# Optimization experiments

Hardware: AMD Instinct MI355X
Metric: run time of the kernel (lower is better)

## Reference

```python
import jax, jax.numpy as jnp
import numpy as np

N = 50000        # nodes
E = 800000       # edges
G = 256          # graphs in batch
NUM_EMB = 100    # atomic number vocab
D = 64           # atom_emb_dim (node channel dim, constant across layers)
ED = 50          # edge_dim
H = 128          # hidden_dim
L = 4            # num_conv_layers
Z = 2 * D + ED   # CGConv concat dim = 178


def setup_inputs() -> dict:
    key = jax.random.key(0)
    ks = jax.random.split(key, 12)
    x = jax.random.randint(ks[0], (N,), 0, NUM_EMB)
    edge_index = jax.random.randint(ks[1], (2, E), 0, N)
    edge_attr = jax.random.normal(ks[2], (E, ED), dtype=jnp.float32)
    batch = jnp.sort(jax.random.randint(ks[3], (N,), 0, G))
    emb = jax.random.normal(ks[4], (NUM_EMB, D), dtype=jnp.float32) * 0.1
    Wf = jax.random.normal(ks[5], (L, Z, D), dtype=jnp.float32) * (Z ** -0.5)
    bf = jnp.zeros((L, D), jnp.float32)
    Ws = jax.random.normal(ks[6], (L, Z, D), dtype=jnp.float32) * (Z ** -0.5)
    bs = jnp.zeros((L, D), jnp.float32)
    W1 = jax.random.normal(ks[7], (D, H), dtype=jnp.float32) * (D ** -0.5)
    b1 = jnp.zeros((H,), jnp.float32)
    W2 = jax.random.normal(ks[8], (H, H // 2), dtype=jnp.float32) * (H ** -0.5)
    b2 = jnp.zeros((H // 2,), jnp.float32)
    Wo = jax.random.normal(ks[9], (H // 2, 1), dtype=jnp.float32) * ((H // 2) ** -0.5)
    bo = jnp.zeros((1,), jnp.float32)
    return dict(x=x, edge_index=edge_index, edge_attr=edge_attr, batch=batch,
                emb=emb, Wf=Wf, bf=bf, Ws=Ws, bs=bs,
                W1=W1, b1=b1, W2=W2, b2=b2, Wo=Wo, bo=bo)


def reference(x, edge_index, edge_attr, batch, emb, Wf, bf, Ws, bs, W1, b1, W2, b2, Wo, bo):
    src = edge_index[0]  # x_j (source / neighbor)
    dst = edge_index[1]  # x_i (target, aggregation index) -- PyG convention
    h = emb[x]           # [N, D]
    for l in range(L):
        # CGConv message: z = [x_i, x_j, e_ij]; gated message; scatter-add; residual
        z = jnp.concatenate([h[dst], h[src], edge_attr], axis=-1)   # [E, Z]
        msg = jax.nn.sigmoid(z @ Wf[l] + bf[l]) * jax.nn.softplus(z @ Ws[l] + bs[l])  # [E, D]
        agg = jax.ops.segment_sum(msg, dst, num_segments=N)          # [N, D]
        h = jax.nn.softplus(h + agg)                                 # residual + F.softplus
    # global mean pool over graphs
    counts = jax.ops.segment_sum(jnp.ones((N, 1), h.dtype), batch, num_segments=G)
    pooled = jax.ops.segment_sum(h, batch, num_segments=G) / jnp.maximum(counts, 1.0)  # [G, D]
    g = jax.nn.relu(pooled @ W1 + b1)   # dropout is identity in eval mode
    g = jax.nn.relu(g @ W2 + b2)
    return (g @ Wo + bo).reshape(-1)    # [G]
```

## Files before the change

kernel.cpp:

```cpp
#include <hip/hip_runtime.h>
#include <hip/hip_bf16.h>
#include <hip/hip_fp16.h>
#include <math.h>

#define N_NODES 50000
#define N_EDGES 800000
#define N_GRAPHS 256
#define DIM 64
#define EDIM 50
#define HDIM 128
#define NLAYER 4
#define ZDIM (2 * DIM + EDIM)
#define NTILES (N_EDGES / 32)

typedef _Float16 f16;
typedef __attribute__((ext_vector_type(4))) _Float16 half4v;
typedef __attribute__((ext_vector_type(8))) _Float16 half8v;
typedef __attribute__((ext_vector_type(16))) float f32x16;

__device__ __forceinline__ float softplus_f(float x) {
    return fmaxf(x, 0.0f) + log1pf(__expf(-fabsf(x)));
}

__device__ __forceinline__ float sigx(float x) {
    float t = __builtin_amdgcn_exp2f(-1.44269504f * x);
    return __builtin_amdgcn_rcpf(1.0f + t);
}
__device__ __forceinline__ float spx(float y) {
    float t = __builtin_amdgcn_exp2f(-1.44269504f * fabsf(y));
    return fmaxf(y, 0.0f) + 0.69314718f * __builtin_amdgcn_logf(1.0f + t);
}

__global__ void k_wprep(const float* __restrict__ Wf, const float* __restrict__ Ws,
                        f16* __restrict__ wcat, f16* __restrict__ wnode) {
    int i = blockIdx.x * 256 + threadIdx.x;
    if (i < 32768) {
        int l = i >> 13;
        int rem = i & 8191;
        int k = rem >> 7;
        int colv = rem & 127;
        int g = colv >> 6, d = colv & 63;
        float v = 0.0f;
        if (k < 50) {
            const float* W = g ? Ws : Wf;
            v = W[((size_t)l * ZDIM + 128 + k) * 64 + d];
        }
        wcat[i] = (f16)v;
    } else {
        int j = i - 32768;
        int l = j >> 14;
        int rem = j & 16383;
        int colv2 = rem >> 6;
        int k = rem & 63;
        int half = colv2 >> 7, g = (colv2 >> 6) & 1, d = colv2 & 63;
        const float* W = g ? Ws : Wf;
        wnode[j] = (f16)W[((size_t)l * ZDIM + half * 64 + k) * 64 + d];
    }
}

__global__ void k_hist(const int* __restrict__ eidx, int* __restrict__ hist) {
    int e = blockIdx.x * 256 + threadIdx.x;
    atomicAdd(&hist[eidx[N_EDGES + e]], 1);
}

__global__ __launch_bounds__(256) void k_scan1(const int* __restrict__ hist,
                                               int* __restrict__ scanbuf,
                                               int* __restrict__ blocksums) {
    int tid = threadIdx.x;
    int i = blockIdx.x * 256 + tid;
    int v = (i < N_NODES) ? hist[i] : 0;
    int lane = tid & 63;
#pragma unroll
    for (int off = 1; off < 64; off <<= 1) {
        int u = __shfl_up(v, off);
        if (lane >= off) v += u;
    }
    __shared__ int wsum[4];
    if (lane == 63) wsum[tid >> 6] = v;
    __syncthreads();
    int w = tid >> 6;
    int add = 0;
#pragma unroll
    for (int k = 0; k < 3; ++k)
        if (k < w) add += wsum[k];
    v += add;
    if (i < N_NODES) scanbuf[i] = v;
    if (tid == 255) blocksums[blockIdx.x] = v;
}

__global__ __launch_bounds__(256) void k_scan2(int* __restrict__ blocksums, int nb) {
    int tid = threadIdx.x;
    int v = (tid < nb) ? blocksums[tid] : 0;
    int lane = tid & 63;
#pragma unroll
    for (int off = 1; off < 64; off <<= 1) {
        int u = __shfl_up(v, off);
        if (lane >= off) v += u;
    }
    __shared__ int wsum[4];
    if (lane == 63) wsum[tid >> 6] = v;
    __syncthreads();
    int w = tid >> 6;
    int add = 0;
#pragma unroll
    for (int k = 0; k < 3; ++k)
        if (k < w) add += wsum[k];
    v += add;
    if (tid < nb) blocksums[tid] = v;
}

__global__ void k_scan3(const int* __restrict__ scanbuf, const int* __restrict__ hist,
                        const int* __restrict__ blocksums, int* __restrict__ cursor) {
    int i = blockIdx.x * 256 + threadIdx.x;
    if (i >= N_NODES) return;
    int b = blockIdx.x;
    int off = b ? blocksums[b - 1] : 0;
    cursor[i] = scanbuf[i] - hist[i] + off;
}

__global__ __launch_bounds__(256) void k_scatter2(
    const int* __restrict__ eidx, const float* __restrict__ eattr,
    int* __restrict__ cursor, int* __restrict__ permSrc, int* __restrict__ permDst,
    f16* __restrict__ eattrP) {
    int e = blockIdx.x * 256 + threadIdx.x;
    int dst = eidx[N_EDGES + e];
    int src = eidx[e];
    int pos = atomicAdd(&cursor[dst], 1);
    permDst[pos] = dst;
    permSrc[pos] = src;

    const float* erow = eattr + (size_t)e * EDIM;
    float ev[50];
#pragma unroll
    for (int k = 0; k < 25; ++k) {
        float2 v = *(const float2*)(erow + 2 * k);
        ev[2 * k] = v.x;
        ev[2 * k + 1] = v.y;
    }
    int tile = pos >> 5, c = pos & 31;
#pragma unroll
    for (int h2 = 0; h2 < 2; ++h2) {
        unsigned lane = (unsigned)(h2 * 32 + c);
#pragma unroll
        for (int kk = 0; kk < 4; ++kk) {
            half8v o;
#pragma unroll
            for (int j = 0; j < 8; ++j) {
                int k = kk * 16 + 8 * h2 + j;
                o[j] = (k < EDIM) ? (f16)ev[k] : (f16)0.0f;
            }
            *(half8v*)&eattrP[(((unsigned)tile * 4u + kk) * 64u + lane) * 8u] = o;
        }
    }
}

template <int MODE>
__global__ __launch_bounds__(256) void k_nodemm(
    const float* __restrict__ hin, float* __restrict__ hout, float* __restrict__ agg,
    const int* __restrict__ x, const float* __restrict__ emb,
    const float* __restrict__ bf, const float* __restrict__ bs,
    const f16* __restrict__ wnode_l,
    __half* __restrict__ dstpack, __half* __restrict__ srcpack) {
    __shared__ f16 hsf[64 * 68];
    int tid = threadIdx.x;
    int w = tid >> 6, lane = tid & 63;
    int c = lane & 31, h2 = lane >> 5;
    int n0 = blockIdx.x * 64;
    for (int idx = tid; idx < 64 * 64; idx += 256) {
        int i = idx >> 6, k = idx & 63;
        int n = n0 + i;
        float v = 0.0f;
        if (n < N_NODES) {
            if (MODE == 1) {
                v = softplus_f(hin[(size_t)n * DIM + k] + agg[(size_t)n * DIM + k]);
                agg[(size_t)n * DIM + k] = 0.0f;
                hout[(size_t)n * DIM + k] = v;
            } else {
                v = emb[x[n] * DIM + k];
                hout[(size_t)n * DIM + k] = v;
            }
        }
        hsf[i * 68 + k] = (f16)v;
    }
    __syncthreads();

    half8v bfr[2][4];
#pragma unroll
    for (int nt = 0; nt < 2; ++nt) {
#pragma unroll
        for (int kk = 0; kk < 4; ++kk) {
            bfr[nt][kk] = *(const half8v*)(wnode_l + ((64 * w + 32 * nt + c) * 64 + kk * 16 + 8 * h2));
        }
    }
    float bias[2];
#pragma unroll
    for (int nt = 0; nt < 2; ++nt) {
        int d = 32 * nt + c;
        bias[nt] = (w == 0) ? bf[d] : (w == 1) ? bs[d] : 0.0f;
    }

    f32x16 acc[2][2];
#pragma unroll
    for (int mt = 0; mt < 2; ++mt)
#pragma unroll
        for (int nt = 0; nt < 2; ++nt)
#pragma unroll
            for (int i = 0; i < 16; ++i) acc[mt][nt][i] = 0.0f;

#pragma unroll
    for (int mt = 0; mt < 2; ++mt) {
        half8v afr[4];
#pragma unroll
        for (int kk = 0; kk < 4; ++kk) {
            const f16* ap = &hsf[(32 * mt + c) * 68 + kk * 16 + 8 * h2];
            half8v a;
            *(half4v*)&a = *(const half4v*)ap;
            *((half4v*)&a + 1) = *(const half4v*)(ap + 4);
            afr[kk] = a;
        }
#pragma unroll
        for (int nt = 0; nt < 2; ++nt)
#pragma unroll
            for (int kk = 0; kk < 4; ++kk)
                acc[mt][nt] = __builtin_amdgcn_mfma_f32_32x32x16_f16(afr[kk], bfr[nt][kk],
                                                                     acc[mt][nt], 0, 0, 0);
    }

    __half* outp = (w < 2) ? dstpack : srcpack;
    int colbase = (w & 1) * 64;
#pragma unroll
    for (int mt = 0; mt < 2; ++mt) {
#pragma unroll
        for (int nt = 0; nt < 2; ++nt) {
#pragma unroll
            for (int r = 0; r < 16; ++r) {
                int row = 32 * mt + (r & 3) + 8 * (r >> 2) + 4 * h2;
                int n = n0 + row;
                if (n < N_NODES) {
                    outp[(size_t)n * 128 + colbase + 32 * nt + c] =
                        __float2half(acc[mt][nt][r] + bias[nt]);
                }
            }
        }
    }
}

__global__ __launch_bounds__(256) void k_edge_s(
    const int* __restrict__ permSrc, const int* __restrict__ permDst,
    const f16* __restrict__ eattrP, const __half* __restrict__ dstpack,
    const __half* __restrict__ srcpack, const f16* __restrict__ wcat_l,
    float* __restrict__ agg) {
    __shared__ float msgV[2][64][34];
    __shared__ int dsh[32];
    int tid = threadIdx.x;
    int w = tid >> 6;
    int lane = tid & 63;
    int c = lane & 31;
    int h2 = lane >> 5;
    int col = w * 32 + c;

    half8v wfr[4];
#pragma unroll
    for (int kk = 0; kk < 4; ++kk) {
#pragma unroll
        for (int e = 0; e < 8; ++e) {
            wfr[kk][e] = wcat_l[(kk * 16 + 8 * h2 + e) * 128 + col];
        }
    }

    for (int tile = blockIdx.x; tile < NTILES; tile += gridDim.x) {
        int e0 = tile * 32;
        int tI = permDst[e0 + c];
        int sI = permSrc[e0 + c];
        if (tid < 32) dsh[tid] = tI;

        half8v efr[4];
        unsigned fb = ((unsigned)tile * 4u) * 64u + (unsigned)lane;
#pragma unroll
        for (int kk = 0; kk < 4; ++kk) {
            efr[kk] = *(const half8v*)&eattrP[(fb + (unsigned)kk * 64u) * 8u];
        }

        f32x16 acc;
#pragma unroll
        for (int i = 0; i < 16; ++i) acc[i] = 0.0f;
#pragma unroll
        for (int kk = 0; kk < 4; ++kk) {
            acc = __builtin_amdgcn_mfma_f32_32x32x16_f16(wfr[kk], efr[kk], acc, 0, 0, 0);
        }

        const __half* drow = dstpack + (((size_t)(unsigned)tI) << 7) + w * 32 + 4 * h2;
        const __half* srow = srcpack + (((size_t)(unsigned)sI) << 7) + w * 32 + 4 * h2;
        float dv[4][4], sv[4][4];
#pragma unroll
        for (int q = 0; q < 4; ++q) {
            const __half2* dp = (const __half2*)(drow + 8 * q);
            float2 lo = __half22float2(dp[0]);
            float2 hi = __half22float2(dp[1]);
            dv[q][0] = lo.x; dv[q][1] = lo.y; dv[q][2] = hi.x; dv[q][3] = hi.y;
        }
#pragma unroll
        for (int q = 0; q < 4; ++q) {
            const __half2* sp = (const __half2*)(srow + 8 * q);
            float2 lo = __half22float2(sp[0]);
            float2 hi = __half22float2(sp[1]);
            sv[q][0] = lo.x; sv[q][1] = lo.y; sv[q][2] = hi.x; sv[q][3] = hi.y;
        }

        int dbase = (w & 1) * 32 + 4 * h2;
        if (w < 2) {
#pragma unroll
            for (int q = 0; q < 4; ++q) {
#pragma unroll
                for (int i = 0; i < 4; ++i) {
                    float pre = acc[4 * q + i] + dv[q][i] + sv[q][i];
                    msgV[0][dbase + 8 * q + i][c] = sigx(pre);
                }
            }
        } else {
#pragma unroll
            for (int q = 0; q < 4; ++q) {
#pragma unroll
                for (int i = 0; i < 4; ++i) {
                    float pre = acc[4 * q + i] + dv[q][i] + sv[q][i];
                    msgV[1][dbase + 8 * q + i][c] = spx(pre);
                }
            }
        }

        __syncthreads();

        {
            int d = tid & 63;
            int base = (tid >> 6) * 8;
            float m[8];
#pragma unroll
            for (int j2 = 0; j2 < 4; ++j2) {
                float2 a = *(const float2*)&msgV[0][d][base + 2 * j2];
                float2 b = *(const float2*)&msgV[1][d][base + 2 * j2];
                m[2 * j2] = a.x * b.x;
                m[2 * j2 + 1] = a.y * b.y;
            }
            float accum = 0.0f;
            int cur = dsh[base];
#pragma unroll
            for (int j = 0; j < 8; ++j) {
                int dn = dsh[base + j];
                if (dn != cur) {
                    unsafeAtomicAdd(&agg[(unsigned)((cur << 6) + d)], accum);
                    accum = 0.0f;
                    cur = dn;
                }
                accum += m[j];
            }
            unsafeAtomicAdd(&agg[(unsigned)((cur << 6) + d)], accum);
        }
        __syncthreads();
    }
}

__global__ __launch_bounds__(256) void k_edge_u(
    const int* __restrict__ eidx, const float* __restrict__ eattr,
    const __half* __restrict__ dstpack, const __half* __restrict__ srcpack,
    const f16* __restrict__ wcat_l, float* __restrict__ agg) {
    __shared__ float msgV[2][32][64];
    __shared__ int dsh[32], ssh[32];
    int tid = threadIdx.x;
    int w = tid >> 6;
    int lane = tid & 63;
    int c = lane & 31;
    int h2 = lane >> 5;
    int col = w * 32 + c;
    int dcol = (w & 1) * 32 + c;

    half8v bfr[4];
#pragma unroll
    for (int kk = 0; kk < 4; ++kk) {
#pragma unroll
        for (int e = 0; e < 8; ++e) bfr[kk][e] = wcat_l[(kk * 16 + 8 * h2 + e) * 128 + col];
    }

    for (int tile = blockIdx.x; tile < NTILES; tile += gridDim.x) {
        int e0 = tile * 32;
        if (lane < 32) {
            dsh[lane] = eidx[N_EDGES + e0 + lane];
            ssh[lane] = eidx[e0 + lane];
        }
        half8v afr[4];
        const float* erow = eattr + (size_t)(e0 + c) * EDIM;
#pragma unroll
        for (int kk = 0; kk < 3; ++kk) {
            int k0 = kk * 16 + 8 * h2;
#pragma unroll
            for (int p = 0; p < 4; ++p) {
                float2 v = *(const float2*)(erow + k0 + 2 * p);
                afr[kk][2 * p] = (f16)v.x;
                afr[kk][2 * p + 1] = (f16)v.y;
            }
        }
        {
            half8v a;
#pragma unroll
            for (int e = 0; e < 8; ++e) a[e] = (f16)0.0f;
            if (h2 == 0) {
                float2 v = *(const float2*)(erow + 48);
                a[0] = (f16)v.x;
                a[1] = (f16)v.y;
            }
            afr[3] = a;
        }
        f32x16 acc;
#pragma unroll
        for (int i = 0; i < 16; ++i) acc[i] = 0.0f;
#pragma unroll
        for (int kk = 0; kk < 4; ++kk)
            acc = __builtin_amdgcn_mfma_f32_32x32x16_f16(afr[kk], bfr[kk], acc, 0, 0, 0);

        __builtin_amdgcn_wave_barrier();

#pragma unroll
        for (int grp = 0; grp < 2; ++grp) {
            int tI[8], sI[8];
            float dv[8], sv[8];
#pragma unroll
            for (int r = 0; r < 8; ++r) {
                int rr = grp * 8 + r;
                int row = (rr & 3) + 8 * (rr >> 2) + 4 * h2;
                tI[r] = dsh[row];
                sI[r] = ssh[row];
            }
#pragma unroll
            for (int r = 0; r < 8; ++r) {
                dv[r] = __half2float(dstpack[(unsigned)((tI[r] << 7) + col)]);
                sv[r] = __half2float(srcpack[(unsigned)((sI[r] << 7) + col)]);
            }
            float pre[8];
#pragma unroll
            for (int r = 0; r < 8; ++r) pre[r] = acc[grp * 8 + r] + dv[r] + sv[r];
            if (w < 2) {
#pragma unroll
                for (int r = 0; r < 8; ++r) {
                    int rr = grp * 8 + r;
                    int row = (rr & 3) + 8 * (rr >> 2) + 4 * h2;
                    msgV[0][row][dcol] = sigx(pre[r]);
                }
            } else {
#pragma unroll
                for (int r = 0; r < 8; ++r) {
                    int rr = grp * 8 + r;
                    int row = (rr & 3) + 8 * (rr >> 2) + 4 * h2;
                    msgV[1][row][dcol] = spx(pre[r]);
                }
            }
        }
        __syncthreads();
        {
            int d = tid & 63;
            int base = (tid >> 6) * 8;
#pragma unroll
            for (int j = 0; j < 8; ++j) {
                int row = base + j;
                float m = msgV[0][row][d] * msgV[1][row][d];
                unsafeAtomicAdd(&agg[(unsigned)((dsh[row] << 6) + d)], m);
            }
        }
        __syncthreads();
    }
}

__global__ __launch_bounds__(256) void k_pool_s(
    const float* __restrict__ h, const float* __restrict__ agg,
    const int* __restrict__ batch,
    float* __restrict__ pooled, float* __restrict__ counts) {
    int tid = threadIdx.x;
    int d = tid & 63;
    int strm = tid >> 6;
    int base = blockIdx.x * 256 + strm * 64;
    if (base >= N_NODES) return;
    int end = min(base + 64, N_NODES);
    float accum = 0.0f;
    int cnt = 0;
    int cur = batch[base];
    for (int n = base; n < end; ++n) {
        int g = batch[n];
        if (g != cur) {
            unsafeAtomicAdd(&pooled[cur * DIM + d], accum);
            if (d == 0) unsafeAtomicAdd(&counts[cur], (float)cnt);
            accum = 0.0f;
            cnt = 0;
            cur = g;
        }
        accum += softplus_f(h[(size_t)n * DIM + d] + agg[(size_t)n * DIM + d]);
        cnt++;
    }
    unsafeAtomicAdd(&pooled[cur * DIM + d], accum);
    if (d == 0) unsafeAtomicAdd(&counts[cur], (float)cnt);
}

__global__ __launch_bounds__(64) void k_mlp(
    const float* __restrict__ pooled, const float* __restrict__ counts,
    const float* __restrict__ W1, const float* __restrict__ b1,
    const float* __restrict__ W2, const float* __restrict__ b2,
    const float* __restrict__ Wo, const float* __restrict__ bo,
    float* __restrict__ out) {
    __shared__ float ps[64];
    __shared__ float h1[128];
    int g = blockIdx.x, lane = threadIdx.x;
    float cnt = fmaxf(counts[g], 1.0f);
    ps[lane] = pooled[g * DIM + lane] / cnt;
    __syncthreads();
#pragma unroll
    for (int rep = 0; rep < 2; ++rep) {
        int j = lane + rep * 64;
        float acc = b1[j];
        for (int k = 0; k < 64; ++k) acc += ps[k] * W1[k * HDIM + j];
        h1[j] = fmaxf(acc, 0.0f);
    }
    __syncthreads();
    float acc = b2[lane];
    for (int k = 0; k < 128; ++k) acc += h1[k] * W2[k * 64 + lane];
    float v = fmaxf(acc, 0.0f) * Wo[lane];
#pragma unroll
    for (int off = 32; off; off >>= 1) v += __shfl_down(v, off);
    if (lane == 0) out[g] = v + bo[0];
}

extern "C" void kernel_launch(void* const* d_in, const int* in_sizes, int n_in,
                              void* d_out, int out_size, void* d_ws, size_t ws_size,
                              hipStream_t stream) {
    const int* x = (const int*)d_in[0];
    const int* eidx = (const int*)d_in[1];
    const float* eattr = (const float*)d_in[2];
    const int* batch = (const int*)d_in[3];
    const float* emb = (const float*)d_in[4];
    const float* Wf = (const float*)d_in[5];
    const float* bf = (const float*)d_in[6];
    const float* Ws = (const float*)d_in[7];
    const float* bs = (const float*)d_in[8];
    const float* W1 = (const float*)d_in[9];
    const float* b1 = (const float*)d_in[10];
    const float* W2 = (const float*)d_in[11];
    const float* b2 = (const float*)d_in[12];
    const float* Wo = (const float*)d_in[13];
    const float* bo = (const float*)d_in[14];
    float* out = (float*)d_out;

    char* p = (char*)d_ws;
    float* h = (float*)p;        p += (size_t)N_NODES * DIM * 4;
    __half* dstpack = (__half*)p; p += (size_t)N_NODES * 2 * DIM * 2;
    __half* srcpack = (__half*)p; p += (size_t)N_NODES * 2 * DIM * 2;
    float* agg = (float*)p;      p += (size_t)N_NODES * DIM * 4;
    float* pooled = (float*)p;   p += (size_t)N_GRAPHS * DIM * 4;
    float* counts = (float*)p;   p += (size_t)N_GRAPHS * 4;
    f16* wcat = (f16*)p;         p += (size_t)NLAYER * 64 * 128 * 2;
    f16* wnode = (f16*)p;        p += (size_t)NLAYER * 256 * 64 * 2;
    f16* eattrP = (f16*)p;       p += (size_t)NTILES * 4 * 64 * 8 * 2;
    int* hist = (int*)p;         p += (size_t)N_NODES * 4;
    int* scanbuf = (int*)p;      p += (size_t)N_NODES * 4;
    int* blocksums = (int*)p;    p += 256 * 4;
    int* cursor = (int*)p;       p += (size_t)N_NODES * 4;
    int* permSrc = (int*)p;      p += (size_t)N_EDGES * 4;
    int* permDst = (int*)p;      p += (size_t)N_EDGES * 4;
    size_t used_sorted = (size_t)(p - (char*)d_ws);

    bool sorted = used_sorted <= ws_size;

    const int SCAN_BLOCKS = (N_NODES + 255) / 256;
    const int NODEMM_BLOCKS = (N_NODES + 63) / 64;

    k_wprep<<<(32768 + 65536) / 256, 256, 0, stream>>>(Wf, Ws, wcat, wnode);
    if (sorted) {
        hipMemsetAsync(hist, 0, (size_t)N_NODES * 4, stream);
        k_hist<<<N_EDGES / 256, 256, 0, stream>>>(eidx, hist);
        k_scan1<<<SCAN_BLOCKS, 256, 0, stream>>>(hist, scanbuf, blocksums);
        k_scan2<<<1, 256, 0, stream>>>(blocksums, SCAN_BLOCKS);
        k_scan3<<<SCAN_BLOCKS, 256, 0, stream>>>(scanbuf, hist, blocksums, cursor);
        k_scatter2<<<N_EDGES / 256, 256, 0, stream>>>(eidx, eattr, cursor,
                                                      permSrc, permDst, eattrP);
    }
    hipMemsetAsync(agg, 0,
                   (size_t)N_NODES * DIM * 4 + (size_t)N_GRAPHS * DIM * 4 + N_GRAPHS * 4,
                   stream);
    for (int l = 0; l < NLAYER; ++l) {
        const f16* wnl = wnode + (size_t)l * 256 * 64;
        if (l == 0) {
            k_nodemm<2><<<NODEMM_BLOCKS, 256, 0, stream>>>(
                nullptr, h, nullptr, x, emb, bf + l * DIM, bs + l * DIM, wnl,
                dstpack, srcpack);
        } else {
            k_nodemm<1><<<NODEMM_BLOCKS, 256, 0, stream>>>(
                h, h, agg, nullptr, nullptr, bf + l * DIM, bs + l * DIM, wnl,
                dstpack, srcpack);
        }
        if (sorted) {
            k_edge_s<<<2048, 256, 0, stream>>>(permSrc, permDst, eattrP, dstpack, srcpack,
                                               wcat + (size_t)l * 64 * 128, agg);
        } else {
            k_edge_u<<<2048, 256, 0, stream>>>(eidx, eattr, dstpack, srcpack,
                                               wcat + (size_t)l * 64 * 128, agg);
        }
    }
    k_pool_s<<<(N_NODES + 255) / 256, 256, 0, stream>>>(h, agg, batch, pooled, counts);
    k_mlp<<<N_GRAPHS, 64, 0, stream>>>(pooled, counts, W1, b1, W2, b2, Wo, bo, out);
}
```

Measured before the change: 691.1 us.

## Split edge-attr packing from scatter and gather attrs via permutation in edge kernel

The scatter kernel now only writes the permutation, src and dst indices. A separate coalesced kernel converts edge attributes to f16 rows of 64 in original edge order. The per-layer edge kernel then gathers each edge's attribute row through the perm array instead of reading a pre-packed tile layout. This aims to make preprocessing cheaper and more coalesced, but it adds random 128-byte gathers and an extra index load in every one of the four edge layers.

```diff
diff --git a/kernel.cpp b/kernel.cpp
--- a/kernel.cpp
+++ b/kernel.cpp
@@ -118,40 +118,22 @@
     cursor[i] = scanbuf[i] - hist[i] + off;
 }
 
-__global__ __launch_bounds__(256) void k_scatter2(
-    const int* __restrict__ eidx, const float* __restrict__ eattr,
-    int* __restrict__ cursor, int* __restrict__ permSrc, int* __restrict__ permDst,
-    f16* __restrict__ eattrP) {
+__global__ void k_scatter(const int* __restrict__ eidx, int* __restrict__ cursor,
+                          int* __restrict__ perm, int* __restrict__ permSrc,
+                          int* __restrict__ permDst) {
     int e = blockIdx.x * 256 + threadIdx.x;
-    int dst = eidx[N_EDGES + e];
-    int src = eidx[e];
-    int pos = atomicAdd(&cursor[dst], 1);
-    permDst[pos] = dst;
-    permSrc[pos] = src;
-
-    const float* erow = eattr + (size_t)e * EDIM;
-    float ev[50];
-#pragma unroll
-    for (int k = 0; k < 25; ++k) {
-        float2 v = *(const float2*)(erow + 2 * k);
-        ev[2 * k] = v.x;
-        ev[2 * k + 1] = v.y;
-    }
-    int tile = pos >> 5, c = pos & 31;
-#pragma unroll
-    for (int h2 = 0; h2 < 2; ++h2) {
-        unsigned lane = (unsigned)(h2 * 32 + c);
-#pragma unroll
-        for (int kk = 0; kk < 4; ++kk) {
-            half8v o;
-#pragma unroll
-            for (int j = 0; j < 8; ++j) {
-                int k = kk * 16 + 8 * h2 + j;
-                o[j] = (k < EDIM) ? (f16)ev[k] : (f16)0.0f;
-            }
-            *(half8v*)&eattrP[(((unsigned)tile * 4u + kk) * 64u + lane) * 8u] = o;
-        }
-    }
+    int d = eidx[N_EDGES + e];
+    int pos = atomicAdd(&cursor[d], 1);
+    perm[pos] = e;
+    permDst[pos] = d;
+    permSrc[pos] = eidx[e];
+}
+
+__global__ void k_eprep3(const float* __restrict__ eattr, f16* __restrict__ eattrP) {
+    int i = blockIdx.x * 256 + threadIdx.x;
+    int edge = i >> 6, k = i & 63;
+    float v = (k < EDIM) ? eattr[(size_t)edge * EDIM + k] : 0.0f;
+    eattrP[i] = (f16)v;
 }
 
 template <int MODE>
@@ -246,7 +228,8 @@
 }
 
 __global__ __launch_bounds__(256) void k_edge_s(
-    const int* __restrict__ permSrc, const int* __restrict__ permDst,
+    const int* __restrict__ perm, const int* __restrict__ permSrc,
+    const int* __restrict__ permDst,
     const f16* __restrict__ eattrP, const __half* __restrict__ dstpack,
     const __half* __restrict__ srcpack, const f16* __restrict__ wcat_l,
     float* __restrict__ agg) {
@@ -272,13 +255,14 @@
         int e0 = tile * 32;
         int tI = permDst[e0 + c];
         int sI = permSrc[e0 + c];
+        int pe = perm[e0 + c];
         if (tid < 32) dsh[tid] = tI;
 
         half8v efr[4];
-        unsigned fb = ((unsigned)tile * 4u) * 64u + (unsigned)lane;
+        const f16* ebase = eattrP + ((size_t)(unsigned)pe << 6) + 8 * h2;
 #pragma unroll
         for (int kk = 0; kk < 4; ++kk) {
-            efr[kk] = *(const half8v*)&eattrP[(fb + (unsigned)kk * 64u) * 8u];
+            efr[kk] = *(const half8v*)(ebase + kk * 16);
         }
 
         f32x16 acc;
@@ -554,11 +538,12 @@
     float* counts = (float*)p;   p += (size_t)N_GRAPHS * 4;
     f16* wcat = (f16*)p;         p += (size_t)NLAYER * 64 * 128 * 2;
     f16* wnode = (f16*)p;        p += (size_t)NLAYER * 256 * 64 * 2;
-    f16* eattrP = (f16*)p;       p += (size_t)NTILES * 4 * 64 * 8 * 2;
+    f16* eattrP = (f16*)p;       p += (size_t)N_EDGES * 64 * 2;
     int* hist = (int*)p;         p += (size_t)N_NODES * 4;
     int* scanbuf = (int*)p;      p += (size_t)N_NODES * 4;
     int* blocksums = (int*)p;    p += 256 * 4;
     int* cursor = (int*)p;       p += (size_t)N_NODES * 4;
+    int* perm = (int*)p;         p += (size_t)N_EDGES * 4;
     int* permSrc = (int*)p;      p += (size_t)N_EDGES * 4;
     int* permDst = (int*)p;      p += (size_t)N_EDGES * 4;
     size_t used_sorted = (size_t)(p - (char*)d_ws);
@@ -575,8 +560,8 @@
         k_scan1<<<SCAN_BLOCKS, 256, 0, stream>>>(hist, scanbuf, blocksums);
         k_scan2<<<1, 256, 0, stream>>>(blocksums, SCAN_BLOCKS);
         k_scan3<<<SCAN_BLOCKS, 256, 0, stream>>>(scanbuf, hist, blocksums, cursor);
-        k_scatter2<<<N_EDGES / 256, 256, 0, stream>>>(eidx, eattr, cursor,
-                                                      permSrc, permDst, eattrP);
+        k_scatter<<<N_EDGES / 256, 256, 0, stream>>>(eidx, cursor, perm, permSrc, permDst);
+        k_eprep3<<<(N_EDGES * 64) / 256, 256, 0, stream>>>(eattr, eattrP);
     }
     hipMemsetAsync(agg, 0,
                    (size_t)N_NODES * DIM * 4 + (size_t)N_GRAPHS * DIM * 4 + N_GRAPHS * 4,
@@ -593,7 +578,8 @@
                 dstpack, srcpack);
         }
         if (sorted) {
-            k_edge_s<<<2048, 256, 0, stream>>>(permSrc, permDst, eattrP, dstpack, srcpack,
+            k_edge_s<<<2048, 256, 0, stream>>>(perm, permSrc, permDst, eattrP,
+                                               dstpack, srcpack,
                                                wcat + (size_t)l * 64 * 128, agg);
         } else {
             k_edge_u<<<2048, 256, 0, stream>>>(eidx, eattr, dstpack, srcpack,
```

After: 838.5 us. +21.3%, slower.
